# Kernel tuning notes

Hardware: AMD Instinct MI355X
Metric: run time of the kernel (lower is better)

Reference implementation:

```python
import jax, jax.numpy as jnp
import numpy as np

T, N, C, D, K = 512, 256, 128, 128, 128

def setup_inputs() -> dict:
    key = jax.random.key(0)
    ks = jax.random.split(key, 6)
    s = 1.0 / np.sqrt(D)
    return {
        "x":   jax.random.normal(ks[0], (T, N, C), dtype=jnp.float32),
        "W_x": jax.random.normal(ks[1], (D, C), dtype=jnp.float32) * s,  # torch Linear: (out,in)
        "b_x": jax.random.normal(ks[2], (D,), dtype=jnp.float32) * s,
        "W_h": jax.random.normal(ks[3], (D, D), dtype=jnp.float32) * s,
        "W_y": jax.random.normal(ks[4], (K, D), dtype=jnp.float32) * s,
        "b_y": jax.random.normal(ks[5], (K,), dtype=jnp.float32) * s,
    }

def reference(x, W_x, b_x, W_h, W_y, b_y):
    # Elman RNN: h_t = relu(x_t @ W_x^T + b_x + h_{t-1} @ W_h^T)
    # Precompute the input projection for all timesteps in one big GEMM,
    # then scan only the true recurrent dependency.
    xproj = jnp.einsum('tnc,dc->tnd', x, W_x) + b_x  # (T, N, D)

    def step(h, xp_t):
        h_new = jax.nn.relu(xp_t + h @ W_h.T)  # (N, D)
        return h_new, h_new

    h0 = jnp.zeros((x.shape[1], W_h.shape[0]), dtype=x.dtype)
    _, all_h = jax.lax.scan(step, h0, xproj)          # (T, N, D)
    all_y = jnp.einsum('tnd,kd->tnk', all_h, W_y) + b_y  # (T, N, K)
    return all_y, all_h
```

## Files before the change

### kernel.cpp

```cpp
#include <hip/hip_runtime.h>

static constexpr int T_STEPS = 512;
static constexpr int NBATCH  = 256;
static constexpr int DD      = 128;
static constexpr long TND    = (long)T_STEPS * NBATCH * DD;

typedef short bf16x8 __attribute__((ext_vector_type(8)));
typedef float f32x4  __attribute__((ext_vector_type(4)));

__device__ inline unsigned short f2bf(float f) {
  unsigned u = __builtin_bit_cast(unsigned, f);
  unsigned r = u + 0x7FFFu + ((u >> 16) & 1u);
  return (unsigned short)(r >> 16);
}

__device__ inline bf16x8 pack8(const float* s) {
  bf16x8 v;
#pragma unroll
  for (int i = 0; i < 8; ++i) v[i] = (short)f2bf(s[i]);
  return v;
}

__global__ __launch_bounds__(256) void gemm128_mfma(
    const float* __restrict__ A, const float* __restrict__ W,
    const float* __restrict__ bias, float* __restrict__ O, int ntiles) {
  const int lane = threadIdx.x & 63;
  const int wib  = threadIdx.x >> 6;
  const int m    = lane & 15;
  const int q    = lane >> 4;

  bf16x8 Wf[8][4];
#pragma unroll
  for (int j = 0; j < 8; ++j)
#pragma unroll
    for (int kq = 0; kq < 4; ++kq) {
      const float* p = W + (j * 16 + m) * DD + kq * 32 + q * 8;
      float t[8];
      *(float4*)&t[0] = *(const float4*)p;
      *(float4*)&t[4] = *(const float4*)(p + 4);
      Wf[j][kq] = pack8(t);
    }
  float bv[8];
#pragma unroll
  for (int j = 0; j < 8; ++j) bv[j] = bias[j * 16 + m];

  const int wglobal = blockIdx.x * 4 + wib;
  const int nwaves  = gridDim.x * 4;
  for (int tile = wglobal; tile < ntiles; tile += nwaves) {
    const long r0 = (long)tile * 16;
    f32x4 acc[8];
#pragma unroll
    for (int j = 0; j < 8; ++j) acc[j] = (f32x4){0.f, 0.f, 0.f, 0.f};

#pragma unroll
    for (int kq = 0; kq < 4; ++kq) {
      const float* p = A + (r0 + m) * DD + kq * 32 + q * 8;
      float t[8];
      *(float4*)&t[0] = *(const float4*)p;
      *(float4*)&t[4] = *(const float4*)(p + 4);
      bf16x8 af = pack8(t);
#pragma unroll
      for (int j = 0; j < 8; ++j)
        acc[j] = __builtin_amdgcn_mfma_f32_16x16x32_bf16(af, Wf[j][kq], acc[j], 0, 0, 0);
    }
#pragma unroll
    for (int j = 0; j < 8; ++j)
#pragma unroll
      for (int r = 0; r < 4; ++r)
        O[(r0 + q * 4 + r) * DD + j * 16 + m] = acc[j][r] + bv[j];
  }
}

__global__ __launch_bounds__(128) void rnn_scan(
    const float* __restrict__ Wh, float* __restrict__ H ) {
  const int tid = threadIdx.x;
  const int jc  = tid & 3;
  const int c   = tid >> 2;
  const int n   = blockIdx.x;

  float w[4][32];
#pragma unroll
  for (int s = 0; s < 4; ++s)
#pragma unroll
    for (int qq = 0; qq < 8; ++qq) {
      float4 wv = *(const float4*)(Wh + (4 * c + s) * DD + jc * 32 + qq * 4);
      w[s][qq * 4 + 0] = wv.x; w[s][qq * 4 + 1] = wv.y;
      w[s][qq * 4 + 2] = wv.z; w[s][qq * 4 + 3] = wv.w;
    }

  __shared__ __align__(16) float hb[2][144];
  for (int i = tid; i < 2 * 144; i += 128) (&hb[0][0])[i] = 0.f;

  const long step = (long)NBATCH * DD;
  float* base = H + (long)n * DD + 4 * c;

  float4 xpb[8], xpn[8];
#pragma unroll
  for (int i = 0; i < 8; ++i) xpb[i] = *(const float4*)(base + (long)i * step);
  __syncthreads();

  int p = 0;
#pragma unroll 1
  for (int ch = 0; ch < 64; ++ch) {
    const long tn0 = (ch < 63) ? (long)(ch + 1) * 8 : 63L * 8;
#pragma unroll
    for (int i = 0; i < 8; ++i) xpn[i] = *(const float4*)(base + (tn0 + i) * step);

    float4 hsv[8];
#pragma unroll
    for (int ti = 0; ti < 8; ++ti) {
      float a0 = 0.f, a1 = 0.f, a2 = 0.f, a3 = 0.f;
#pragma unroll
      for (int qq = 0; qq < 8; ++qq) {
        float4 h4 = *(const float4*)&hb[p][jc * 36 + qq * 4];
        a0 += h4.x * w[0][qq*4] + h4.y * w[0][qq*4+1] + h4.z * w[0][qq*4+2] + h4.w * w[0][qq*4+3];
        a1 += h4.x * w[1][qq*4] + h4.y * w[1][qq*4+1] + h4.z * w[1][qq*4+2] + h4.w * w[1][qq*4+3];
        a2 += h4.x * w[2][qq*4] + h4.y * w[2][qq*4+1] + h4.z * w[2][qq*4+2] + h4.w * w[2][qq*4+3];
        a3 += h4.x * w[3][qq*4] + h4.y * w[3][qq*4+1] + h4.z * w[3][qq*4+2] + h4.w * w[3][qq*4+3];
      }
      a0 += __shfl_xor(a0, 1); a0 += __shfl_xor(a0, 2);
      a1 += __shfl_xor(a1, 1); a1 += __shfl_xor(a1, 2);
      a2 += __shfl_xor(a2, 1); a2 += __shfl_xor(a2, 2);
      a3 += __shfl_xor(a3, 1); a3 += __shfl_xor(a3, 2);

      if (jc == 0) {
        float4 hv;
        hv.x = fmaxf(a0 + xpb[ti].x, 0.f);
        hv.y = fmaxf(a1 + xpb[ti].y, 0.f);
        hv.z = fmaxf(a2 + xpb[ti].z, 0.f);
        hv.w = fmaxf(a3 + xpb[ti].w, 0.f);
        const int pos = 4 * c + 4 * (c >> 3);
        *(float4*)&hb[p ^ 1][pos] = hv;
        hsv[ti] = hv;
      }
      __syncthreads();
      p ^= 1;
    }

    if (jc == 0) {
#pragma unroll
      for (int ti = 0; ti < 8; ++ti)
        *(float4*)(base + (long)(ch * 8 + ti) * step) = hsv[ti];
    }
#pragma unroll
    for (int i = 0; i < 8; ++i) xpb[i] = xpn[i];
  }
}

extern "C" void kernel_launch(void* const* d_in, const int* in_sizes, int n_in,
                              void* d_out, int out_size, void* d_ws, size_t ws_size,
                              hipStream_t stream) {
  const float* x  = (const float*)d_in[0];
  const float* Wx = (const float*)d_in[1];
  const float* bx = (const float*)d_in[2];
  const float* Wh = (const float*)d_in[3];
  const float* Wy = (const float*)d_in[4];
  const float* by = (const float*)d_in[5];

  float* Y = (float*)d_out;
  float* H = (float*)d_out + TND;

  const int ntiles = T_STEPS * NBATCH / 16;

  gemm128_mfma<<<512, 256, 0, stream>>>(x, Wx, bx, H, ntiles);
  rnn_scan<<<NBATCH, 128, 0, stream>>>(Wh, H);
  gemm128_mfma<<<512, 256, 0, stream>>>(H, Wy, by, Y, ntiles);
}
```

Before: 561.3 us.

## Rewrite recurrent scan with bf16 MFMA, one wave per 16 batch rows

Replaces the per-batch FP32 scalar scan (128 threads, LDS ping-pong plus a block barrier every step) with a single-wave kernel. Each wave owns 16 batch rows and computes each step as MFMA with W_h held in registers as bf16. The new hidden state is repacked in registers into the next step's B operand, so no LDS or barriers are needed, and xproj loads are prefetched four steps ahead. The cost is only 16 waves of parallelism and bf16 rounding of h in the recurrence, which can compound error across 512 steps.

```diff
diff --git a/kernel.cpp b/kernel.cpp
--- a/kernel.cpp
+++ b/kernel.cpp
@@ -7,6 +7,7 @@
 
 typedef short bf16x8 __attribute__((ext_vector_type(8)));
 typedef float f32x4  __attribute__((ext_vector_type(4)));
+typedef unsigned u32x4 __attribute__((ext_vector_type(4)));
 
 __device__ inline unsigned short f2bf(float f) {
   unsigned u = __builtin_bit_cast(unsigned, f);
@@ -19,6 +20,12 @@
 #pragma unroll
   for (int i = 0; i < 8; ++i) v[i] = (short)f2bf(s[i]);
   return v;
+}
+
+__device__ __forceinline__ unsigned cvtpk_bf16(float lo, float hi) {
+  unsigned r;
+  asm("v_cvt_pk_bf16_f32 %0, %1, %2" : "=v"(r) : "v"(lo), "v"(hi));
+  return r;
 }
 
 __global__ __launch_bounds__(256) void gemm128_mfma(
@@ -71,79 +78,72 @@
   }
 }
 
-__global__ __launch_bounds__(128) void rnn_scan(
+__global__ __launch_bounds__(64, 1) void rnn_scan_mfma(
     const float* __restrict__ Wh, float* __restrict__ H ) {
-  const int tid = threadIdx.x;
-  const int jc  = tid & 3;
-  const int c   = tid >> 2;
-  const int n   = blockIdx.x;
+  const int lane = threadIdx.x & 63;
+  const int m = lane & 15;
+  const int q = lane >> 4;
 
-  float w[4][32];
+  bf16x8 Whf[8][4];
 #pragma unroll
-  for (int s = 0; s < 4; ++s)
+  for (int j = 0; j < 8; ++j)
 #pragma unroll
-    for (int qq = 0; qq < 8; ++qq) {
-      float4 wv = *(const float4*)(Wh + (4 * c + s) * DD + jc * 32 + qq * 4);
-      w[s][qq * 4 + 0] = wv.x; w[s][qq * 4 + 1] = wv.y;
-      w[s][qq * 4 + 2] = wv.z; w[s][qq * 4 + 3] = wv.w;
+    for (int kq = 0; kq < 4; ++kq) {
+      const float* p = Wh + (j * 16 + m) * DD + kq * 32 + 4 * q;
+      float t[8];
+      *(float4*)&t[0] = *(const float4*)p;
+      *(float4*)&t[4] = *(const float4*)(p + 16);
+      Whf[j][kq] = pack8(t);
     }
 
-  __shared__ __align__(16) float hb[2][144];
-  for (int i = tid; i < 2 * 144; i += 128) (&hb[0][0])[i] = 0.f;
+  const long stepN = (long)NBATCH * DD;
+  float* base = H + (long)(blockIdx.x * 16 + m) * DD + 4 * q;
 
-  const long step = (long)NBATCH * DD;
-  float* base = H + (long)n * DD + 4 * c;
+  unsigned w[8][2];
+#pragma unroll
+  for (int j = 0; j < 8; ++j) { w[j][0] = 0u; w[j][1] = 0u; }
 
-  float4 xpb[8], xpn[8];
+  auto pref = [&](f32x4 (&xp)[8], int t) {
+    const float* pp = base + (long)t * stepN;
 #pragma unroll
-  for (int i = 0; i < 8; ++i) xpb[i] = *(const float4*)(base + (long)i * step);
-  __syncthreads();
+    for (int j = 0; j < 8; ++j) xp[j] = *(const f32x4*)(pp + j * 16);
+  };
 
-  int p = 0;
+  auto step = [&](const f32x4 (&xp)[8], int t) {
+    f32x4 acc[8];
+#pragma unroll
+    for (int j = 0; j < 8; ++j) acc[j] = xp[j];
+#pragma unroll
+    for (int kq = 0; kq < 4; ++kq) {
+      u32x4 bw;
+      bw[0] = w[2 * kq][0];     bw[1] = w[2 * kq][1];
+      bw[2] = w[2 * kq + 1][0]; bw[3] = w[2 * kq + 1][1];
+      bf16x8 bf = __builtin_bit_cast(bf16x8, bw);
+#pragma unroll
+      for (int j = 0; j < 8; ++j)
+        acc[j] = __builtin_amdgcn_mfma_f32_16x16x32_bf16(Whf[j][kq], bf, acc[j], 0, 0, 0);
+    }
+    float* hp = base + (long)t * stepN;
+#pragma unroll
+    for (int j = 0; j < 8; ++j) {
+      f32x4 hv;
+#pragma unroll
+      for (int r = 0; r < 4; ++r) hv[r] = fmaxf(acc[j][r], 0.f);
+      w[j][0] = cvtpk_bf16(hv[0], hv[1]);
+      w[j][1] = cvtpk_bf16(hv[2], hv[3]);
+      *(f32x4*)(hp + j * 16) = hv;
+    }
+  };
+
+  f32x4 xA[8], xB[8], xC[8], xD[8];
+  pref(xA, 0); pref(xB, 1); pref(xC, 2); pref(xD, 3);
+
 #pragma unroll 1
-  for (int ch = 0; ch < 64; ++ch) {
-    const long tn0 = (ch < 63) ? (long)(ch + 1) * 8 : 63L * 8;
-#pragma unroll
-    for (int i = 0; i < 8; ++i) xpn[i] = *(const float4*)(base + (tn0 + i) * step);
-
-    float4 hsv[8];
-#pragma unroll
-    for (int ti = 0; ti < 8; ++ti) {
-      float a0 = 0.f, a1 = 0.f, a2 = 0.f, a3 = 0.f;
-#pragma unroll
-      for (int qq = 0; qq < 8; ++qq) {
-        float4 h4 = *(const float4*)&hb[p][jc * 36 + qq * 4];
-        a0 += h4.x * w[0][qq*4] + h4.y * w[0][qq*4+1] + h4.z * w[0][qq*4+2] + h4.w * w[0][qq*4+3];
-        a1 += h4.x * w[1][qq*4] + h4.y * w[1][qq*4+1] + h4.z * w[1][qq*4+2] + h4.w * w[1][qq*4+3];
-        a2 += h4.x * w[2][qq*4] + h4.y * w[2][qq*4+1] + h4.z * w[2][qq*4+2] + h4.w * w[2][qq*4+3];
-        a3 += h4.x * w[3][qq*4] + h4.y * w[3][qq*4+1] + h4.z * w[3][qq*4+2] + h4.w * w[3][qq*4+3];
-      }
-      a0 += __shfl_xor(a0, 1); a0 += __shfl_xor(a0, 2);
-      a1 += __shfl_xor(a1, 1); a1 += __shfl_xor(a1, 2);
-      a2 += __shfl_xor(a2, 1); a2 += __shfl_xor(a2, 2);
-      a3 += __shfl_xor(a3, 1); a3 += __shfl_xor(a3, 2);
-
-      if (jc == 0) {
-        float4 hv;
-        hv.x = fmaxf(a0 + xpb[ti].x, 0.f);
-        hv.y = fmaxf(a1 + xpb[ti].y, 0.f);
-        hv.z = fmaxf(a2 + xpb[ti].z, 0.f);
-        hv.w = fmaxf(a3 + xpb[ti].w, 0.f);
-        const int pos = 4 * c + 4 * (c >> 3);
-        *(float4*)&hb[p ^ 1][pos] = hv;
-        hsv[ti] = hv;
-      }
-      __syncthreads();
-      p ^= 1;
-    }
-
-    if (jc == 0) {
-#pragma unroll
-      for (int ti = 0; ti < 8; ++ti)
-        *(float4*)(base + (long)(ch * 8 + ti) * step) = hsv[ti];
-    }
-#pragma unroll
-    for (int i = 0; i < 8; ++i) xpb[i] = xpn[i];
+  for (int t = 0; t < T_STEPS; t += 4) {
+    step(xA, t);     pref(xA, t + 4 < T_STEPS ? t + 4 : T_STEPS - 1);
+    step(xB, t + 1); pref(xB, t + 5 < T_STEPS ? t + 5 : T_STEPS - 1);
+    step(xC, t + 2); pref(xC, t + 6 < T_STEPS ? t + 6 : T_STEPS - 1);
+    step(xD, t + 3); pref(xD, t + 7 < T_STEPS ? t + 7 : T_STEPS - 1);
   }
 }
 
@@ -163,6 +163,6 @@
   const int ntiles = T_STEPS * NBATCH / 16;
 
   gemm128_mfma<<<512, 256, 0, stream>>>(x, Wx, bx, H, ntiles);
-  rnn_scan<<<NBATCH, 128, 0, stream>>>(Wh, H);
+  rnn_scan_mfma<<<NBATCH / 16, 64, 0, stream>>>(Wh, H);
   gemm128_mfma<<<512, 256, 0, stream>>>(H, Wy, by, Y, ntiles);
 }
```

New measurement: 542.4 us. -3.4%, faster.
